# Optimization experiments

Hardware: AMD Instinct MI355X
Metric: run time of the kernel (lower is better)

Reference implementation:

```python
import jax, jax.numpy as jnp
import numpy as np

D_MODEL = 128; D_STATE = 64; HEADDIM = 32; D_CONV = 4; EXPAND = 2
D_INNER = EXPAND * D_MODEL          # 256
NHEADS = D_INNER // HEADDIM         # 8
NGROUPS = 1
D_CONV_CH = D_INNER + 2 * NGROUPS * D_STATE      # 384
D_IN_PROJ = 2 * D_INNER + 2 * NGROUPS * D_STATE + NHEADS  # 648


def _mamba2(u, Win, convw, convb, dtb, Alog, Dp, normw, Wout):
    # u: (B, L, d_model). Mamba2 forward (ngroups=1, rmsnorm gated, no in/out bias).
    B, L, _ = u.shape
    zxbcdt = u @ Win                                   # (B,L,648)
    z, xBC, dt = jnp.split(zxbcdt, [D_INNER, D_INNER + D_CONV_CH], axis=-1)
    # depthwise causal conv1d (kernel D_CONV) + SiLU
    xp = jnp.pad(xBC, ((0, 0), (D_CONV - 1, 0), (0, 0)))
    xconv = sum(xp[:, k:k + L, :] * convw[k] for k in range(D_CONV)) + convb
    xBC = jax.nn.silu(xconv)
    x, Bm, Cm = jnp.split(xBC, [D_INNER, D_INNER + NGROUPS * D_STATE], axis=-1)
    dt = jax.nn.softplus(dt + dtb)                     # (B,L,H)
    A = -jnp.exp(Alog)                                 # (H,)
    xh = x.reshape(B, L, NHEADS, HEADDIM)              # (B,L,H,P)
    dA = jnp.exp(dt * A)                               # (B,L,H)

    def step(h, inp):
        dA_t, dt_t, B_t, C_t, x_t = inp
        h = h * dA_t[:, :, None, None] + jnp.einsum('bh,bn,bhp->bhpn', dt_t, B_t, x_t)
        y = jnp.einsum('bhpn,bn->bhp', h, C_t)
        return h, y

    h0 = jnp.zeros((B, NHEADS, HEADDIM, D_STATE), dtype=u.dtype)
    xs = (jnp.moveaxis(dA, 1, 0), jnp.moveaxis(dt, 1, 0), jnp.moveaxis(Bm, 1, 0),
          jnp.moveaxis(Cm, 1, 0), jnp.moveaxis(xh, 1, 0))
    _, ys = jax.lax.scan(step, h0, xs)
    y = jnp.moveaxis(ys, 0, 1) + Dp[None, None, :, None] * xh   # skip D
    y = y.reshape(B, L, D_INNER)
    # RMSNormGated (norm_before_gate=False): rmsnorm(y * silu(z)) * weight
    y = y * jax.nn.silu(z)
    y = y * jax.lax.rsqrt(jnp.mean(y * y, axis=-1, keepdims=True) + 1e-5) * normw
    return y @ Wout


def _cross_attn(x, ctx, Wq, bq, Wk, bk, Wv, bv, Wo, bo):
    Q = x @ Wq + bq
    K = ctx @ Wk + bk
    V = ctx @ Wv + bv
    att = jax.nn.softmax(jnp.einsum('bqd,bkd->bqk', Q, K) * (D_MODEL ** -0.5), axis=-1)
    return jnp.einsum('bqk,bkd->bqd', att, V) @ Wo + bo


def setup_inputs() -> dict:
    key = jax.random.key(0)
    ks = jax.random.split(key, 8)
    B, L = 2048, 8

    def lin(k, fi, fo):
        return jax.random.normal(k, (fi, fo), jnp.float32) / np.sqrt(fi)

    def mamba_params(kseq):
        k = jax.random.split(kseq, 6)
        dt = jax.random.uniform(k[3], (NHEADS,), minval=0.001, maxval=0.1)
        return {
            'Win': lin(k[0], D_MODEL, D_IN_PROJ),
            'convw': jax.random.normal(k[1], (D_CONV, D_CONV_CH), jnp.float32) * 0.2,
            'convb': jnp.zeros((D_CONV_CH,), jnp.float32),
            'dtb': dt + jnp.log(-jnp.expm1(-dt)),  # inverse softplus
            'Alog': jnp.log(jax.random.uniform(k[4], (NHEADS,), minval=1.0, maxval=16.0)),
            'D': jnp.ones((NHEADS,), jnp.float32),
            'normw': jnp.ones((D_INNER,), jnp.float32),
            'Wout': lin(k[5], D_INNER, D_MODEL),
        }

    inp = {
        'st_feature': jax.random.normal(ks[0], (B, L, D_MODEL), jnp.float32),
        'exp_feature': jax.random.normal(ks[1], (B, L, D_MODEL), jnp.float32),
    }
    for pref, p in (('st_', mamba_params(ks[2])), ('ex_', mamba_params(ks[3]))):
        for n, v in p.items():
            inp[pref + n] = v

    def ca(kseq, pref):
        k = jax.random.split(kseq, 4)
        d = {}
        for n, kk in zip(('Wq', 'Wk', 'Wv', 'Wo'), k):
            d[pref + n] = lin(kk, D_MODEL, D_MODEL)
            d[pref + 'b' + n[1]] = jnp.zeros((D_MODEL,), jnp.float32)
        return d

    inp.update(ca(ks[4], 'cx_'))  # cross_atten_exp
    inp.update(ca(ks[5], 'cs_'))  # cross_atten_st
    inp['mlp_W'] = lin(ks[6], 8 * 2 * D_MODEL, 1024)
    inp['mlp_b'] = jnp.zeros((1024,), jnp.float32)
    return inp


def reference(st_feature, exp_feature,
              st_Win, st_convw, st_convb, st_dtb, st_Alog, st_D, st_normw, st_Wout,
              ex_Win, ex_convw, ex_convb, ex_dtb, ex_Alog, ex_D, ex_normw, ex_Wout,
              cx_Wq, cx_bq, cx_Wk, cx_bk, cx_Wv, cx_bv, cx_Wo, cx_bo,
              cs_Wq, cs_bq, cs_Wk, cs_bk, cs_Wv, cs_bv, cs_Wo, cs_bo,
              mlp_W, mlp_b):
    exp_f = _mamba2(exp_feature, ex_Win, ex_convw, ex_convb, ex_dtb, ex_Alog, ex_D, ex_normw, ex_Wout)
    st_f = _mamba2(st_feature, st_Win, st_convw, st_convb, st_dtb, st_Alog, st_D, st_normw, st_Wout)
    exp_a = _cross_attn(exp_f, st_f, cx_Wq, cx_bq, cx_Wk, cx_bk, cx_Wv, cx_bv, cx_Wo, cx_bo)
    st_a = _cross_attn(st_f, exp_f, cs_Wq, cs_bq, cs_Wk, cs_bk, cs_Wv, cs_bv, cs_Wo, cs_bo)
    x = jnp.concatenate([st_a, exp_a], axis=-1)        # (B, 8, 256)
    x = x.reshape(x.shape[0], -1)                      # (B, 2048)
    return x @ mlp_W + mlp_b
```

## Files before the change

kernel.cpp:

```cpp
#include <hip/hip_runtime.h>
#include <hip/hip_bf16.h>
#include <math.h>

#define B_SZ 2048
#define L_SEQ 8
#define DMODEL 128
#define DSTATE 64
#define HEADDIM 32
#define DCONV 4
#define DINNER 256
#define NHEADS 8
#define DCONVCH 384
#define DINPROJ 648
#define NPAD 656

typedef short bf16x8 __attribute__((ext_vector_type(8)));
typedef float floatx4 __attribute__((ext_vector_type(4)));

__device__ __forceinline__ float siluf(float x) {
    return x / (1.f + expf(-x));
}
__device__ __forceinline__ float bf2f(unsigned short h) {
    unsigned int u = ((unsigned int)h) << 16;
    return __builtin_bit_cast(float, u);
}
__device__ __forceinline__ unsigned short f2bf(float f) {
    __hip_bfloat16 b = __float2bfloat16(f);
    return __builtin_bit_cast(unsigned short, b);
}
__device__ __forceinline__ void unpack8(bf16x8 v, float* o) {
    #pragma unroll
    for (int j = 0; j < 8; ++j) o[j] = bf2f((unsigned short)v[j]);
}
__device__ __forceinline__ void gl_lds16(const unsigned short* g, unsigned short* l) {
    __builtin_amdgcn_global_load_lds(
        (const __attribute__((address_space(1))) unsigned int*)g,
        (__attribute__((address_space(3))) unsigned int*)l, 16, 0, 0);
}

__global__ __launch_bounds__(256) void prep_weights(
    const float* __restrict__ st_Win, const float* __restrict__ ex_Win,
    const float* __restrict__ st_Wout, const float* __restrict__ ex_Wout,
    const float* __restrict__ st_normw, const float* __restrict__ ex_normw,
    const float* __restrict__ cs_Wq, const float* __restrict__ cs_Wk,
    const float* __restrict__ cs_Wv, const float* __restrict__ cs_Wo,
    const float* __restrict__ cx_Wq, const float* __restrict__ cx_Wk,
    const float* __restrict__ cx_Wv, const float* __restrict__ cx_Wo,
    unsigned short* __restrict__ winT_st, unsigned short* __restrict__ winT_ex,
    unsigned short* __restrict__ woutT_st, unsigned short* __restrict__ woutT_ex,
    unsigned short* __restrict__ attnWT)
{
    int blk = blockIdx.x;
    if (blk < 656) {
        const float* src = blk < 328 ? st_Win : ex_Win;
        unsigned short* dst = blk < 328 ? winT_st : winT_ex;
        int idx = (blk % 328) * 256 + threadIdx.x;
        if (idx >= NPAD * 128) return;
        int n = idx / 128, k = idx % 128;
        float v = (n < DINPROJ) ? src[k * DINPROJ + n] : 0.f;
        dst[idx] = f2bf(v);
    } else if (blk < 912) {
        const float* src = blk < 784 ? st_Wout : ex_Wout;
        const float* nw  = blk < 784 ? st_normw : ex_normw;
        unsigned short* dst = blk < 784 ? woutT_st : woutT_ex;
        int idx = ((blk - 656) % 128) * 256 + threadIdx.x;
        int n = idx / 256, k = idx % 256;
        dst[idx] = f2bf(src[k * 128 + n] * nw[k]);
    } else {
        int b2 = blk - 912;
        int mat = b2 >> 6;
        const float* src = mat == 0 ? cs_Wq : mat == 1 ? cs_Wk : mat == 2 ? cs_Wv :
                           mat == 3 ? cs_Wo : mat == 4 ? cx_Wq : mat == 5 ? cx_Wk :
                           mat == 6 ? cx_Wv : cx_Wo;
        int e = (b2 & 63) * 256 + threadIdx.x;
        int n = e >> 7, k = e & 127;
        attnWT[mat * 16384 + n * 128 + k] = f2bf(src[k * 128 + n]);
    }
}

#define LDK 136
#define LDZ 648
__global__ __launch_bounds__(256, 3) void mamba_dual(
    const float* __restrict__ u_ex, const float* __restrict__ u_st,
    const unsigned short* __restrict__ WinT_ex, const unsigned short* __restrict__ WinT_st,
    const float* __restrict__ convw_ex, const float* __restrict__ convw_st,
    const float* __restrict__ convb_ex, const float* __restrict__ convb_st,
    const float* __restrict__ dtb_ex, const float* __restrict__ dtb_st,
    const float* __restrict__ Alog_ex, const float* __restrict__ Alog_st,
    const float* __restrict__ Dp_ex, const float* __restrict__ Dp_st,
    const unsigned short* __restrict__ WoutT_ex, const unsigned short* __restrict__ WoutT_st,
    unsigned short* __restrict__ out_ex, unsigned short* __restrict__ out_st,
    const float* __restrict__ mlp_W, unsigned short* __restrict__ mlpWt)
{
    const int tid = threadIdx.x;

    __shared__ __align__(16) unsigned short uA[32 * LDK];
    __shared__ __align__(16) unsigned short zx[32 * LDZ];
    __shared__ float dtv[4][8][8];
    __shared__ float cum[4][8][8];
    __shared__ float Gm[4][8][8];

    if (blockIdx.x >= 1024) {
        int b2 = blockIdx.x - 1024;
        int n0 = (b2 & 31) * 32, k0 = (b2 >> 5) * 32;
        float* tile = (float*)uA;
        const int c = tid & 31, r0 = tid >> 5;
        for (int rr = r0; rr < 32; rr += 8)
            tile[rr * 33 + c] = mlp_W[(size_t)(k0 + rr) * 1024 + n0 + c];
        __syncthreads();
        for (int rr = r0; rr < 32; rr += 8)
            mlpWt[(size_t)(n0 + rr) * 2048 + k0 + c] = f2bf(tile[c * 33 + rr]);
        return;
    }

    const int which = blockIdx.x >> 9;
    const float* u = which ? u_st : u_ex;
    const unsigned short* WinT = which ? WinT_st : WinT_ex;
    const float* convw = which ? convw_st : convw_ex;
    const float* convb = which ? convb_st : convb_ex;
    const float* dtb = which ? dtb_st : dtb_ex;
    const float* Alog = which ? Alog_st : Alog_ex;
    const float* Dp = which ? Dp_st : Dp_ex;
    const unsigned short* WoutT = which ? WoutT_st : WoutT_ex;
    unsigned short* outf = which ? out_st : out_ex;

    const int lane = tid & 63;
    const int wave = tid >> 6;
    const int l15 = lane & 15;
    const int q8 = (lane >> 4) * 8;
    const int row0 = (lane >> 4) * 4;
    const int grow0 = (blockIdx.x & 511) * 32;

    float* coefp = (float*)uA;
    float* rstdp = coefp + 2048;

    #pragma unroll
    for (int it = 0; it < 4; ++it) {
        int i = tid + it * 256;
        int r = i >> 5, k4 = (i & 31) * 4;
        float4 v = *(const float4*)(u + (size_t)(grow0 + r) * DMODEL + k4);
        ushort4 h;
        h.x = f2bf(v.x); h.y = f2bf(v.y); h.z = f2bf(v.z); h.w = f2bf(v.w);
        *(ushort4*)(uA + r * LDK + k4) = h;
    }
    __syncthreads();

    {
        bf16x8 af[2][4];
        #pragma unroll
        for (int mt = 0; mt < 2; ++mt)
            #pragma unroll
            for (int kk = 0; kk < 4; ++kk)
                af[mt][kk] = *(const bf16x8*)(uA + (mt * 16 + l15) * LDK + kk * 32 + q8);
        for (int j = wave; j < 82; j += 4) {
            int mt = (j >= 41) ? 1 : 0;
            int nt = j - mt * 41;
            floatx4 acc = {0.f, 0.f, 0.f, 0.f};
            const unsigned short* bp = WinT + (size_t)(nt * 16 + l15) * 128 + q8;
            #pragma unroll
            for (int kk = 0; kk < 4; ++kk) {
                bf16x8 bf = *(const bf16x8*)(bp + kk * 32);
                acc = __builtin_amdgcn_mfma_f32_16x16x32_bf16(af[mt][kk], bf, acc, 0, 0, 0);
            }
            if (nt == 40) {
                if (l15 < 8) {
                    float dbv = dtb[l15];
                    #pragma unroll
                    for (int r = 0; r < 4; ++r) {
                        int rr = mt * 16 + row0 + r;
                        float v = acc[r] + dbv;
                        dtv[rr >> 3][rr & 7][l15] = (v > 20.f) ? v : log1pf(expf(v));
                    }
                }
            } else {
                #pragma unroll
                for (int r = 0; r < 4; ++r)
                    zx[(mt * 16 + row0 + r) * LDZ + nt * 16 + l15] = f2bf(acc[r]);
            }
        }
    }
    __syncthreads();

    float cv[6][8];
    {
        #pragma unroll
        for (int it = 0; it < 6; ++it) {
            int i = tid + it * 256;
            int r = i / 48, g = i % 48;
            int c0 = g * 8;
            int l = r & 7, bloc = r >> 3;
            float s[8];
            float4 cb0 = *(const float4*)(convb + c0);
            float4 cb1 = *(const float4*)(convb + c0 + 4);
            s[0] = cb0.x; s[1] = cb0.y; s[2] = cb0.z; s[3] = cb0.w;
            s[4] = cb1.x; s[5] = cb1.y; s[6] = cb1.z; s[7] = cb1.w;
            #pragma unroll
            for (int k = 0; k < DCONV; ++k) {
                int lp = l + k - (DCONV - 1);
                if (lp >= 0) {
                    bf16x8 v = *(const bf16x8*)(zx + (bloc * 8 + lp) * LDZ + 256 + c0);
                    float vf[8];
                    unpack8(v, vf);
                    float4 w0 = *(const float4*)(convw + k * DCONVCH + c0);
                    float4 w1 = *(const float4*)(convw + k * DCONVCH + c0 + 4);
                    s[0] += vf[0] * w0.x; s[1] += vf[1] * w0.y;
                    s[2] += vf[2] * w0.z; s[3] += vf[3] * w0.w;
                    s[4] += vf[4] * w1.x; s[5] += vf[5] * w1.y;
                    s[6] += vf[6] * w1.z; s[7] += vf[7] * w1.w;
                }
            }
            #pragma unroll
            for (int j = 0; j < 8; ++j) cv[it][j] = siluf(s[j]);
        }
    }
    __syncthreads();
    {
        #pragma unroll
        for (int it = 0; it < 6; ++it) {
            int i = tid + it * 256;
            int r = i / 48, c0 = (i % 48) * 8;
            bf16x8 o;
            #pragma unroll
            for (int j = 0; j < 8; ++j) o[j] = (short)f2bf(cv[it][j]);
            *(bf16x8*)(zx + r * LDZ + 256 + c0) = o;
        }
        if (tid < 32) {
            int bloc = tid >> 3, h = tid & 7;
            float c = 0.f;
            for (int l = 0; l < L_SEQ; ++l) { c += dtv[bloc][l][h]; cum[bloc][l][h] = c; }
        }
    }
    __syncthreads();

    {
        int bloc = tid >> 6, t = (tid >> 3) & 7, s = tid & 7;
        float a = 0.f;
        #pragma unroll
        for (int n = 0; n < DSTATE; n += 8) {
            bf16x8 bv = *(const bf16x8*)(zx + (bloc * 8 + s) * LDZ + 512 + n);
            bf16x8 cvv = *(const bf16x8*)(zx + (bloc * 8 + t) * LDZ + 576 + n);
            float bf_[8], cf_[8];
            unpack8(bv, bf_); unpack8(cvv, cf_);
            #pragma unroll
            for (int j = 0; j < 8; ++j) a += bf_[j] * cf_[j];
        }
        Gm[bloc][t][s] = a;
    }
    __syncthreads();

    #pragma unroll
    for (int it = 0; it < 8; ++it) {
        int i = tid + it * 256;
        int bloc = i >> 9, t = (i >> 6) & 7, s = (i >> 3) & 7, h = i & 7;
        float A = -expf(Alog[h]);
        coefp[i] = (s <= t)
            ? Gm[bloc][t][s] * expf(A * (cum[bloc][t][h] - cum[bloc][s][h])) * dtv[bloc][s][h]
            : 0.f;
    }
    __syncthreads();

    float pj[4];
    bf16x8 yo[4];
    int rF[4], c0F[4];
    {
        #pragma unroll
        for (int it = 0; it < 4; ++it) {
            int i = tid + it * 256;
            int r = i >> 5, g = i & 31;
            int c0 = g * 8, h = g >> 2;
            int bloc = r >> 3, t = r & 7;
            float acc[8];
            {
                bf16x8 xv = *(const bf16x8*)(zx + r * LDZ + 256 + c0);
                float xf[8]; unpack8(xv, xf);
                float d = Dp[h];
                #pragma unroll
                for (int j = 0; j < 8; ++j) acc[j] = d * xf[j];
            }
            for (int s = 0; s <= t; ++s) {
                float cf = coefp[((bloc * 8 + t) * 8 + s) * 8 + h];
                bf16x8 xv = *(const bf16x8*)(zx + (bloc * 8 + s) * LDZ + 256 + c0);
                float xf[8]; unpack8(xv, xf);
                #pragma unroll
                for (int j = 0; j < 8; ++j) acc[j] += cf * xf[j];
            }
            bf16x8 zv = *(const bf16x8*)(zx + r * LDZ + c0);
            float zf[8]; unpack8(zv, zf);
            float p = 0.f;
            #pragma unroll
            for (int j = 0; j < 8; ++j) {
                float y = acc[j] * siluf(zf[j]);
                p += y * y;
                yo[it][j] = (short)f2bf(y);
            }
            pj[it] = p; rF[it] = r; c0F[it] = c0;
        }
    }
    #pragma unroll
    for (int m = 1; m < 32; m <<= 1) {
        #pragma unroll
        for (int it = 0; it < 4; ++it) pj[it] += __shfl_xor(pj[it], m);
    }
    if ((tid & 31) == 0) {
        #pragma unroll
        for (int it = 0; it < 4; ++it)
            rstdp[rF[it]] = rsqrtf(pj[it] * (1.f / 256.f) + 1e-5f);
    }
    __syncthreads();
    #pragma unroll
    for (int it = 0; it < 4; ++it)
        *(bf16x8*)(zx + rF[it] * LDZ + 256 + c0F[it]) = yo[it];
    __syncthreads();

    {
        bf16x8 af[2][8];
        #pragma unroll
        for (int mt = 0; mt < 2; ++mt)
            #pragma unroll
            for (int kk = 0; kk < 8; ++kk)
                af[mt][kk] = *(const bf16x8*)(zx + (mt * 16 + l15) * LDZ + 256 + kk * 32 + q8);
        #pragma unroll
        for (int ni = 0; ni < 2; ++ni) {
            int nt = wave * 2 + ni;
            const unsigned short* bp = WoutT + (size_t)(nt * 16 + l15) * 256 + q8;
            bf16x8 bfr[8];
            #pragma unroll
            for (int kk = 0; kk < 8; ++kk) bfr[kk] = *(const bf16x8*)(bp + kk * 32);
            #pragma unroll
            for (int mt = 0; mt < 2; ++mt) {
                floatx4 acc = {0.f, 0.f, 0.f, 0.f};
                #pragma unroll
                for (int kk = 0; kk < 8; ++kk)
                    acc = __builtin_amdgcn_mfma_f32_16x16x32_bf16(af[mt][kk], bfr[kk], acc, 0, 0, 0);
                #pragma unroll
                for (int r = 0; r < 4; ++r) {
                    int rr = mt * 16 + row0 + r;
                    outf[(size_t)(grow0 + rr) * DMODEL + nt * 16 + l15] =
                        f2bf(acc[r] * rstdp[rr]);
                }
            }
        }
    }
}

#define ASTR 136
#define VSTR 40
#define PSTR 40
__global__ __launch_bounds__(256, 2) void attn_kernel(
    const unsigned short* __restrict__ st_f,
    const unsigned short* __restrict__ exp_f,
    const unsigned short* __restrict__ WT,
    const float* __restrict__ cs_bq, const float* __restrict__ cs_bk,
    const float* __restrict__ cs_bv, const float* __restrict__ cs_bo,
    const float* __restrict__ cx_bq, const float* __restrict__ cx_bk,
    const float* __restrict__ cx_bv, const float* __restrict__ cx_bo,
    __hip_bfloat16* __restrict__ x)
{
    const int tid = threadIdx.x;
    const int lane = tid & 63, wave = tid >> 6;
    const int l15 = lane & 15;
    const int q8 = (lane >> 4) * 8;
    const int row0 = (lane >> 4) * 4;
    const int grow0 = blockIdx.x * 32;
    const int b0 = blockIdx.x * 4;
    const float scale = 0.08838834764831845f;

    __shared__ __align__(16) unsigned short stf[32 * ASTR];
    __shared__ __align__(16) unsigned short exf[32 * ASTR];
    __shared__ __align__(16) unsigned short Qs[32 * ASTR];
    __shared__ __align__(16) unsigned short Ks[32 * ASTR];
    __shared__ __align__(16) unsigned short attv[32 * ASTR];
    __shared__ __align__(16) unsigned short Vt[128 * VSTR];
    __shared__ __align__(16) unsigned short P[32 * PSTR];
    __shared__ float Ss[32][33];

    #pragma unroll
    for (int it = 0; it < 2; ++it) {
        int i = tid + it * 256;
        int r = i >> 4, c8 = (i & 15) * 8;
        *(uint4*)(stf + r * ASTR + c8) = *(const uint4*)(st_f + (size_t)(grow0 + r) * 128 + c8);
        *(uint4*)(exf + r * ASTR + c8) = *(const uint4*)(exp_f + (size_t)(grow0 + r) * 128 + c8);
    }
    __syncthreads();

    #pragma unroll
    for (int pass = 0; pass < 2; ++pass) {
        const unsigned short* qsrc = pass ? exf : stf;
        const unsigned short* kvsrc = pass ? stf : exf;
        const unsigned short* Wq = WT + (size_t)pass * 4 * 16384;
        const unsigned short* Wk = Wq + 16384;
        const unsigned short* Wv = Wq + 32768;
        const unsigned short* Wo = Wq + 49152;
        const float* bq = pass ? cx_bq : cs_bq;
        const float* bk = pass ? cx_bk : cs_bk;
        const float* bv = pass ? cx_bv : cs_bv;
        const float* bo = pass ? cx_bo : cs_bo;

        {
            bf16x8 aq[2][4], akv[2][4];
            #pragma unroll
            for (int mt = 0; mt < 2; ++mt)
                #pragma unroll
                for (int kk = 0; kk < 4; ++kk) {
                    aq[mt][kk]  = *(const bf16x8*)(qsrc  + (mt * 16 + l15) * ASTR + kk * 32 + q8);
                    akv[mt][kk] = *(const bf16x8*)(kvsrc + (mt * 16 + l15) * ASTR + kk * 32 + q8);
                }
            #pragma unroll
            for (int ni = 0; ni < 2; ++ni) {
                int nc = (wave * 2 + ni) * 16 + l15;
                floatx4 aq0 = {0,0,0,0}, aq1 = {0,0,0,0};
                floatx4 ak0 = {0,0,0,0}, ak1 = {0,0,0,0};
                floatx4 av0 = {0,0,0,0}, av1 = {0,0,0,0};
                #pragma unroll
                for (int kk = 0; kk < 4; ++kk) {
                    bf16x8 wqf = *(const bf16x8*)(Wq + (size_t)nc * 128 + kk * 32 + q8);
                    bf16x8 wkf = *(const bf16x8*)(Wk + (size_t)nc * 128 + kk * 32 + q8);
                    bf16x8 wvf = *(const bf16x8*)(Wv + (size_t)nc * 128 + kk * 32 + q8);
                    aq0 = __builtin_amdgcn_mfma_f32_16x16x32_bf16(aq[0][kk],  wqf, aq0, 0, 0, 0);
                    aq1 = __builtin_amdgcn_mfma_f32_16x16x32_bf16(aq[1][kk],  wqf, aq1, 0, 0, 0);
                    ak0 = __builtin_amdgcn_mfma_f32_16x16x32_bf16(akv[0][kk], wkf, ak0, 0, 0, 0);
                    ak1 = __builtin_amdgcn_mfma_f32_16x16x32_bf16(akv[1][kk], wkf, ak1, 0, 0, 0);
                    av0 = __builtin_amdgcn_mfma_f32_16x16x32_bf16(akv[0][kk], wvf, av0, 0, 0, 0);
                    av1 = __builtin_amdgcn_mfma_f32_16x16x32_bf16(akv[1][kk], wvf, av1, 0, 0, 0);
                }
                float bqv = bq[nc], bkv = bk[nc], bvv = bv[nc];
                #pragma unroll
                for (int r = 0; r < 4; ++r) {
                    Qs[(row0 + r) * ASTR + nc]      = f2bf(aq0[r] + bqv);
                    Qs[(16 + row0 + r) * ASTR + nc] = f2bf(aq1[r] + bqv);
                    Ks[(row0 + r) * ASTR + nc]      = f2bf(ak0[r] + bkv);
                    Ks[(16 + row0 + r) * ASTR + nc] = f2bf(ak1[r] + bkv);
                    Vt[nc * VSTR + row0 + r]        = f2bf(av0[r] + bvv);
                    Vt[nc * VSTR + 16 + row0 + r]   = f2bf(av1[r] + bvv);
                }
            }
        }
        __syncthreads();

        {
            int mtS = wave >> 1, ntS = wave & 1;
            floatx4 s = {0,0,0,0};
            #pragma unroll
            for (int kk = 0; kk < 4; ++kk) {
                bf16x8 a = *(const bf16x8*)(Qs + (mtS * 16 + l15) * ASTR + kk * 32 + q8);
                bf16x8 b = *(const bf16x8*)(Ks + (ntS * 16 + l15) * ASTR + kk * 32 + q8);
                s = __builtin_amdgcn_mfma_f32_16x16x32_bf16(a, b, s, 0, 0, 0);
            }
            #pragma unroll
            for (int r = 0; r < 4; ++r)
                Ss[mtS * 16 + row0 + r][ntS * 16 + l15] = s[r];
        }
        __syncthreads();

        if (tid < 32) {
            int r = tid, c0 = (r >> 3) * 8;
            float v[8], mx = -1e30f;
            #pragma unroll
            for (int c = 0; c < 8; ++c) {
                v[c] = Ss[r][c0 + c] * scale;
                mx = fmaxf(mx, v[c]);
            }
            float sum = 0.f;
            #pragma unroll
            for (int c = 0; c < 8; ++c) { v[c] = expf(v[c] - mx); sum += v[c]; }
            float inv = 1.f / sum;
            #pragma unroll
            for (int c = 0; c < 32; ++c) {
                float pv = (c >= c0 && c < c0 + 8) ? v[c - c0] * inv : 0.f;
                P[r * PSTR + c] = f2bf(pv);
            }
        }
        __syncthreads();

        {
            #pragma unroll
            for (int ni = 0; ni < 2; ++ni) {
                int nc = (wave * 2 + ni) * 16 + l15;
                bf16x8 bv_ = *(const bf16x8*)(Vt + nc * VSTR + q8);
                #pragma unroll
                for (int mt = 0; mt < 2; ++mt) {
                    bf16x8 ap = *(const bf16x8*)(P + (mt * 16 + l15) * PSTR + q8);
                    floatx4 o = {0,0,0,0};
                    o = __builtin_amdgcn_mfma_f32_16x16x32_bf16(ap, bv_, o, 0, 0, 0);
                    #pragma unroll
                    for (int r = 0; r < 4; ++r)
                        attv[(mt * 16 + row0 + r) * ASTR + nc] = f2bf(o[r]);
                }
            }
        }
        __syncthreads();

        {
            bf16x8 ao[2][4];
            #pragma unroll
            for (int mt = 0; mt < 2; ++mt)
                #pragma unroll
                for (int kk = 0; kk < 4; ++kk)
                    ao[mt][kk] = *(const bf16x8*)(attv + (mt * 16 + l15) * ASTR + kk * 32 + q8);
            #pragma unroll
            for (int ni = 0; ni < 2; ++ni) {
                int nc = (wave * 2 + ni) * 16 + l15;
                floatx4 a0 = {0,0,0,0}, a1 = {0,0,0,0};
                #pragma unroll
                for (int kk = 0; kk < 4; ++kk) {
                    bf16x8 wof = *(const bf16x8*)(Wo + (size_t)nc * 128 + kk * 32 + q8);
                    a0 = __builtin_amdgcn_mfma_f32_16x16x32_bf16(ao[0][kk], wof, a0, 0, 0, 0);
                    a1 = __builtin_amdgcn_mfma_f32_16x16x32_bf16(ao[1][kk], wof, a1, 0, 0, 0);
                }
                float bov = bo[nc];
                #pragma unroll
                for (int r = 0; r < 4; ++r) {
                    int rr0 = row0 + r;
                    int rr1 = 16 + row0 + r;
                    x[(size_t)(b0 + (rr0 >> 3)) * 2048 + (rr0 & 7) * 256 + pass * 128 + nc] =
                        __float2bfloat16(a0[r] + bov);
                    x[(size_t)(b0 + (rr1 >> 3)) * 2048 + (rr1 & 7) * 256 + pass * 128 + nc] =
                        __float2bfloat16(a1[r] + bov);
                }
            }
        }
        __syncthreads();
    }
}

__global__ __launch_bounds__(256, 5) void mlp_mfma(
    const unsigned short* __restrict__ X,
    const unsigned short* __restrict__ Wt,
    const float* __restrict__ bias,
    float* __restrict__ out)
{
    __shared__ __align__(16) unsigned short As[2][64 * 64];
    __shared__ __align__(16) unsigned short Bs[2][64 * 64];
    const int tid = threadIdx.x;
    const int wave = tid >> 6, lane = tid & 63;
    const int wm = (wave >> 1) * 32, wn = (wave & 1) * 32;
    const int bm = blockIdx.y * 64, bn = blockIdx.x * 64;
    const int l15 = lane & 15, q8 = (lane >> 4) * 8;

    const int c0i = tid, c1i = tid + 256;
    const int r0s = c0i >> 3, c0s = ((c0i & 7) ^ (r0s & 7)) * 8;
    const int r1s = c1i >> 3, c1s = ((c1i & 7) ^ (r1s & 7)) * 8;
    const unsigned short* gA0 = X + (size_t)(bm + r0s) * 2048 + c0s;
    const unsigned short* gA1 = X + (size_t)(bm + r1s) * 2048 + c1s;
    const unsigned short* gB0 = Wt + (size_t)(bn + r0s) * 2048 + c0s;
    const unsigned short* gB1 = Wt + (size_t)(bn + r1s) * 2048 + c1s;

    floatx4 acc[2][2];
    #pragma unroll
    for (int i = 0; i < 2; ++i)
        #pragma unroll
        for (int j = 0; j < 2; ++j) acc[i][j] = (floatx4){0.f, 0.f, 0.f, 0.f};

    const int ra0 = wm + l15, ra1 = wm + 16 + l15;
    const int rb0 = wn + l15, rb1 = wn + 16 + l15;

    gl_lds16(gA0, As[0] + c0i * 8);
    gl_lds16(gA1, As[0] + c1i * 8);
    gl_lds16(gB0, Bs[0] + c0i * 8);
    gl_lds16(gB1, Bs[0] + c1i * 8);
    __syncthreads();

    int cur = 0;
    for (int t = 0; t < 32; ++t) {
        if (t < 31) {
            int k0 = (t + 1) * 64;
            unsigned short* An = As[cur ^ 1];
            unsigned short* Bn = Bs[cur ^ 1];
            gl_lds16(gA0 + k0, An + c0i * 8);
            gl_lds16(gA1 + k0, An + c1i * 8);
            gl_lds16(gB0 + k0, Bn + c0i * 8);
            gl_lds16(gB1 + k0, Bn + c1i * 8);
        }
        const unsigned short* Ac = As[cur];
        const unsigned short* Bc = Bs[cur];
        #pragma unroll
        for (int ks = 0; ks < 2; ++ks) {
            int xx = ks * 4 + (q8 >> 3);
            bf16x8 a0 = *(const bf16x8*)(Ac + (ra0 * 8 + (xx ^ (ra0 & 7))) * 8);
            bf16x8 a1 = *(const bf16x8*)(Ac + (ra1 * 8 + (xx ^ (ra1 & 7))) * 8);
            bf16x8 b0 = *(const bf16x8*)(Bc + (rb0 * 8 + (xx ^ (rb0 & 7))) * 8);
            bf16x8 b1 = *(const bf16x8*)(Bc + (rb1 * 8 + (xx ^ (rb1 & 7))) * 8);
            acc[0][0] = __builtin_amdgcn_mfma_f32_16x16x32_bf16(a0, b0, acc[0][0], 0, 0, 0);
            acc[0][1] = __builtin_amdgcn_mfma_f32_16x16x32_bf16(a0, b1, acc[0][1], 0, 0, 0);
            acc[1][0] = __builtin_amdgcn_mfma_f32_16x16x32_bf16(a1, b0, acc[1][0], 0, 0, 0);
            acc[1][1] = __builtin_amdgcn_mfma_f32_16x16x32_bf16(a1, b1, acc[1][1], 0, 0, 0);
        }
        __syncthreads();
        cur ^= 1;
    }

    const int row0 = (lane >> 4) * 4;
    #pragma unroll
    for (int j = 0; j < 2; ++j) {
        int col = bn + wn + j * 16 + l15;
        float bv = bias[col];
        #pragma unroll
        for (int r = 0; r < 4; ++r) {
            out[(size_t)(bm + wm + row0 + r) * 1024 + col] = acc[0][j][r] + bv;
            out[(size_t)(bm + wm + 16 + row0 + r) * 1024 + col] = acc[1][j][r] + bv;
        }
    }
}

extern "C" void kernel_launch(void* const* d_in, const int* in_sizes, int n_in,
                              void* d_out, int out_size, void* d_ws, size_t ws_size,
                              hipStream_t stream) {
    const float* st_feature = (const float*)d_in[0];
    const float* exp_feature = (const float*)d_in[1];
    const float* st_Win = (const float*)d_in[2];
    const float* st_convw = (const float*)d_in[3];
    const float* st_convb = (const float*)d_in[4];
    const float* st_dtb = (const float*)d_in[5];
    const float* st_Alog = (const float*)d_in[6];
    const float* st_D = (const float*)d_in[7];
    const float* st_normw = (const float*)d_in[8];
    const float* st_Wout = (const float*)d_in[9];
    const float* ex_Win = (const float*)d_in[10];
    const float* ex_convw = (const float*)d_in[11];
    const float* ex_convb = (const float*)d_in[12];
    const float* ex_dtb = (const float*)d_in[13];
    const float* ex_Alog = (const float*)d_in[14];
    const float* ex_D = (const float*)d_in[15];
    const float* ex_normw = (const float*)d_in[16];
    const float* ex_Wout = (const float*)d_in[17];
    const float* cx_Wq = (const float*)d_in[18]; const float* cx_bq = (const float*)d_in[19];
    const float* cx_Wk = (const float*)d_in[20]; const float* cx_bk = (const float*)d_in[21];
    const float* cx_Wv = (const float*)d_in[22]; const float* cx_bv = (const float*)d_in[23];
    const float* cx_Wo = (const float*)d_in[24]; const float* cx_bo = (const float*)d_in[25];
    const float* cs_Wq = (const float*)d_in[26]; const float* cs_bq = (const float*)d_in[27];
    const float* cs_Wk = (const float*)d_in[28]; const float* cs_bk = (const float*)d_in[29];
    const float* cs_Wv = (const float*)d_in[30]; const float* cs_bv = (const float*)d_in[31];
    const float* cs_Wo = (const float*)d_in[32]; const float* cs_bo = (const float*)d_in[33];
    const float* mlp_W = (const float*)d_in[34];
    const float* mlp_b = (const float*)d_in[35];

    unsigned short* wsu = (unsigned short*)d_ws;
    unsigned short* st_fb  = wsu;
    unsigned short* exp_fb = st_fb + (size_t)B_SZ * L_SEQ * DMODEL;
    unsigned short* xbuf   = exp_fb + (size_t)B_SZ * L_SEQ * DMODEL;
    unsigned short* wtbuf  = xbuf + (size_t)2048 * 2048;
    unsigned short* winT_st = wtbuf + (size_t)1024 * 2048;
    unsigned short* winT_ex = winT_st + (size_t)NPAD * 128;
    unsigned short* woutT_st = winT_ex + (size_t)NPAD * 128;
    unsigned short* woutT_ex = woutT_st + (size_t)128 * 256;
    unsigned short* attnWT  = woutT_ex + (size_t)128 * 256;

    prep_weights<<<1424, 256, 0, stream>>>(
        st_Win, ex_Win, st_Wout, ex_Wout, st_normw, ex_normw,
        cs_Wq, cs_Wk, cs_Wv, cs_Wo, cx_Wq, cx_Wk, cx_Wv, cx_Wo,
        winT_st, winT_ex, woutT_st, woutT_ex, attnWT);
    mamba_dual<<<3072, 256, 0, stream>>>(
        exp_feature, st_feature, winT_ex, winT_st,
        ex_convw, st_convw, ex_convb, st_convb,
        ex_dtb, st_dtb, ex_Alog, st_Alog, ex_D, st_D,
        woutT_ex, woutT_st,
        exp_fb, st_fb,
        mlp_W, wtbuf);
    attn_kernel<<<B_SZ / 4, 256, 0, stream>>>(st_fb, exp_fb, attnWT,
                                              cs_bq, cs_bk, cs_bv, cs_bo,
                                              cx_bq, cx_bk, cx_bv, cx_bo,
                                              (__hip_bfloat16*)xbuf);
    {
        dim3 g(1024 / 64, 2048 / 64);
        mlp_mfma<<<g, 256, 0, stream>>>(xbuf, wtbuf, mlp_b, (float*)d_out);
    }
}
```

Baseline: 260.7 us.

## Fuse cross-attention into Mamba kernel by pairing exp/st rows per block

Each Mamba block now handles 16 rows from the exp stream and the matching 16 rows from the st stream, so both feature sets for two batch items sit in the same block. The cross-attention (QKV projections, scores, softmax, PV and output projection) then runs inside the same kernel on shared memory. This removes the separate attention launch and the global round-trip of both feature buffers. In exchange each block switches weight pointers per half, loads Wout fragments per tile instead of reusing them across both row tiles, and does more serial work, which may raise register pressure.

After: 271.2 us. 1.04x slower.

```diff
diff --git a/kernel.cpp b/kernel.cpp
--- a/kernel.cpp
+++ b/kernel.cpp
@@ -80,7 +80,8 @@
 
 #define LDK 136
 #define LDZ 648
-__global__ __launch_bounds__(256, 3) void mamba_dual(
+#define ASTR 136
+__global__ __launch_bounds__(256, 3) void mamba_attn(
     const float* __restrict__ u_ex, const float* __restrict__ u_st,
     const unsigned short* __restrict__ WinT_ex, const unsigned short* __restrict__ WinT_st,
     const float* __restrict__ convw_ex, const float* __restrict__ convw_st,
@@ -89,7 +90,12 @@
     const float* __restrict__ Alog_ex, const float* __restrict__ Alog_st,
     const float* __restrict__ Dp_ex, const float* __restrict__ Dp_st,
     const unsigned short* __restrict__ WoutT_ex, const unsigned short* __restrict__ WoutT_st,
-    unsigned short* __restrict__ out_ex, unsigned short* __restrict__ out_st,
+    const unsigned short* __restrict__ attnWT,
+    const float* __restrict__ cs_bq, const float* __restrict__ cs_bk,
+    const float* __restrict__ cs_bv, const float* __restrict__ cs_bo,
+    const float* __restrict__ cx_bq, const float* __restrict__ cx_bk,
+    const float* __restrict__ cx_bv, const float* __restrict__ cx_bo,
+    __hip_bfloat16* __restrict__ x,
     const float* __restrict__ mlp_W, unsigned short* __restrict__ mlpWt)
 {
     const int tid = threadIdx.x;
@@ -113,32 +119,25 @@
         return;
     }
 
-    const int which = blockIdx.x >> 9;
-    const float* u = which ? u_st : u_ex;
-    const unsigned short* WinT = which ? WinT_st : WinT_ex;
-    const float* convw = which ? convw_st : convw_ex;
-    const float* convb = which ? convb_st : convb_ex;
-    const float* dtb = which ? dtb_st : dtb_ex;
-    const float* Alog = which ? Alog_st : Alog_ex;
-    const float* Dp = which ? Dp_st : Dp_ex;
-    const unsigned short* WoutT = which ? WoutT_st : WoutT_ex;
-    unsigned short* outf = which ? out_st : out_ex;
-
     const int lane = tid & 63;
     const int wave = tid >> 6;
     const int l15 = lane & 15;
     const int q8 = (lane >> 4) * 8;
     const int row0 = (lane >> 4) * 4;
-    const int grow0 = (blockIdx.x & 511) * 32;
+    const int pairIdx = blockIdx.x;
+    const int grow0 = pairIdx * 16;
+    const int b0 = pairIdx * 2;
 
     float* coefp = (float*)uA;
-    float* rstdp = coefp + 2048;
+    float* rstdp = (float*)Gm;
 
     #pragma unroll
     for (int it = 0; it < 4; ++it) {
         int i = tid + it * 256;
         int r = i >> 5, k4 = (i & 31) * 4;
-        float4 v = *(const float4*)(u + (size_t)(grow0 + r) * DMODEL + k4);
+        const float* usrc = (r < 16) ? (u_ex + (size_t)(grow0 + r) * DMODEL)
+                                     : (u_st + (size_t)(grow0 + r - 16) * DMODEL);
+        float4 v = *(const float4*)(usrc + k4);
         ushort4 h;
         h.x = f2bf(v.x); h.y = f2bf(v.y); h.z = f2bf(v.z); h.w = f2bf(v.w);
         *(ushort4*)(uA + r * LDK + k4) = h;
@@ -155,6 +154,7 @@
         for (int j = wave; j < 82; j += 4) {
             int mt = (j >= 41) ? 1 : 0;
             int nt = j - mt * 41;
+            const unsigned short* WinT = mt ? WinT_st : WinT_ex;
             floatx4 acc = {0.f, 0.f, 0.f, 0.f};
             const unsigned short* bp = WinT + (size_t)(nt * 16 + l15) * 128 + q8;
             #pragma unroll
@@ -164,7 +164,7 @@
             }
             if (nt == 40) {
                 if (l15 < 8) {
-                    float dbv = dtb[l15];
+                    float dbv = (mt ? dtb_st : dtb_ex)[l15];
                     #pragma unroll
                     for (int r = 0; r < 4; ++r) {
                         int rr = mt * 16 + row0 + r;
@@ -189,9 +189,11 @@
             int r = i / 48, g = i % 48;
             int c0 = g * 8;
             int l = r & 7, bloc = r >> 3;
+            const float* cw = (r < 16) ? convw_ex : convw_st;
+            const float* cb = (r < 16) ? convb_ex : convb_st;
             float s[8];
-            float4 cb0 = *(const float4*)(convb + c0);
-            float4 cb1 = *(const float4*)(convb + c0 + 4);
+            float4 cb0 = *(const float4*)(cb + c0);
+            float4 cb1 = *(const float4*)(cb + c0 + 4);
             s[0] = cb0.x; s[1] = cb0.y; s[2] = cb0.z; s[3] = cb0.w;
             s[4] = cb1.x; s[5] = cb1.y; s[6] = cb1.z; s[7] = cb1.w;
             #pragma unroll
@@ -201,8 +203,8 @@
                     bf16x8 v = *(const bf16x8*)(zx + (bloc * 8 + lp) * LDZ + 256 + c0);
                     float vf[8];
                     unpack8(v, vf);
-                    float4 w0 = *(const float4*)(convw + k * DCONVCH + c0);
-                    float4 w1 = *(const float4*)(convw + k * DCONVCH + c0 + 4);
+                    float4 w0 = *(const float4*)(cw + k * DCONVCH + c0);
+                    float4 w1 = *(const float4*)(cw + k * DCONVCH + c0 + 4);
                     s[0] += vf[0] * w0.x; s[1] += vf[1] * w0.y;
                     s[2] += vf[2] * w0.z; s[3] += vf[3] * w0.w;
                     s[4] += vf[4] * w1.x; s[5] += vf[5] * w1.y;
@@ -252,7 +254,7 @@
     for (int it = 0; it < 8; ++it) {
         int i = tid + it * 256;
         int bloc = i >> 9, t = (i >> 6) & 7, s = (i >> 3) & 7, h = i & 7;
-        float A = -expf(Alog[h]);
+        float A = -expf((bloc < 2 ? Alog_ex : Alog_st)[h]);
         coefp[i] = (s <= t)
             ? Gm[bloc][t][s] * expf(A * (cum[bloc][t][h] - cum[bloc][s][h])) * dtv[bloc][s][h]
             : 0.f;
@@ -273,7 +275,7 @@
             {
                 bf16x8 xv = *(const bf16x8*)(zx + r * LDZ + 256 + c0);
                 float xf[8]; unpack8(xv, xf);
-                float d = Dp[h];
+                float d = (bloc < 2 ? Dp_ex : Dp_st)[h];
                 #pragma unroll
                 for (int j = 0; j < 8; ++j) acc[j] = d * xf[j];
             }
@@ -312,6 +314,7 @@
         *(bf16x8*)(zx + rF[it] * LDZ + 256 + c0F[it]) = yo[it];
     __syncthreads();
 
+    unsigned short* fout = uA;
     {
         bf16x8 af[2][8];
         #pragma unroll
@@ -322,204 +325,156 @@
         #pragma unroll
         for (int ni = 0; ni < 2; ++ni) {
             int nt = wave * 2 + ni;
-            const unsigned short* bp = WoutT + (size_t)(nt * 16 + l15) * 256 + q8;
-            bf16x8 bfr[8];
-            #pragma unroll
-            for (int kk = 0; kk < 8; ++kk) bfr[kk] = *(const bf16x8*)(bp + kk * 32);
             #pragma unroll
             for (int mt = 0; mt < 2; ++mt) {
+                const unsigned short* WoutT = mt ? WoutT_st : WoutT_ex;
+                const unsigned short* bp = WoutT + (size_t)(nt * 16 + l15) * 256 + q8;
                 floatx4 acc = {0.f, 0.f, 0.f, 0.f};
                 #pragma unroll
-                for (int kk = 0; kk < 8; ++kk)
-                    acc = __builtin_amdgcn_mfma_f32_16x16x32_bf16(af[mt][kk], bfr[kk], acc, 0, 0, 0);
+                for (int kk = 0; kk < 8; ++kk) {
+                    bf16x8 bf = *(const bf16x8*)(bp + kk * 32);
+                    acc = __builtin_amdgcn_mfma_f32_16x16x32_bf16(af[mt][kk], bf, acc, 0, 0, 0);
+                }
                 #pragma unroll
                 for (int r = 0; r < 4; ++r) {
                     int rr = mt * 16 + row0 + r;
-                    outf[(size_t)(grow0 + rr) * DMODEL + nt * 16 + l15] =
-                        f2bf(acc[r] * rstdp[rr]);
-                }
-            }
-        }
-    }
-}
-
-#define ASTR 136
-#define VSTR 40
-#define PSTR 40
-__global__ __launch_bounds__(256, 2) void attn_kernel(
-    const unsigned short* __restrict__ st_f,
-    const unsigned short* __restrict__ exp_f,
-    const unsigned short* __restrict__ WT,
-    const float* __restrict__ cs_bq, const float* __restrict__ cs_bk,
-    const float* __restrict__ cs_bv, const float* __restrict__ cs_bo,
-    const float* __restrict__ cx_bq, const float* __restrict__ cx_bk,
-    const float* __restrict__ cx_bv, const float* __restrict__ cx_bo,
-    __hip_bfloat16* __restrict__ x)
-{
-    const int tid = threadIdx.x;
-    const int lane = tid & 63, wave = tid >> 6;
-    const int l15 = lane & 15;
-    const int q8 = (lane >> 4) * 8;
-    const int row0 = (lane >> 4) * 4;
-    const int grow0 = blockIdx.x * 32;
-    const int b0 = blockIdx.x * 4;
+                    fout[rr * ASTR + nt * 16 + l15] = f2bf(acc[r] * rstdp[rr]);
+                }
+            }
+        }
+    }
+    __syncthreads();
+
+    unsigned short* Qs  = zx;
+    unsigned short* Ks  = zx + 4352;
+    unsigned short* Vt  = zx + 8704;
+    unsigned short* P   = zx + 13824;
+    float*          Ssf = (float*)(zx + 15104);
+    unsigned short* attv = Qs;
     const float scale = 0.08838834764831845f;
 
-    __shared__ __align__(16) unsigned short stf[32 * ASTR];
-    __shared__ __align__(16) unsigned short exf[32 * ASTR];
-    __shared__ __align__(16) unsigned short Qs[32 * ASTR];
-    __shared__ __align__(16) unsigned short Ks[32 * ASTR];
-    __shared__ __align__(16) unsigned short attv[32 * ASTR];
-    __shared__ __align__(16) unsigned short Vt[128 * VSTR];
-    __shared__ __align__(16) unsigned short P[32 * PSTR];
-    __shared__ float Ss[32][33];
-
-    #pragma unroll
-    for (int it = 0; it < 2; ++it) {
-        int i = tid + it * 256;
-        int r = i >> 4, c8 = (i & 15) * 8;
-        *(uint4*)(stf + r * ASTR + c8) = *(const uint4*)(st_f + (size_t)(grow0 + r) * 128 + c8);
-        *(uint4*)(exf + r * ASTR + c8) = *(const uint4*)(exp_f + (size_t)(grow0 + r) * 128 + c8);
-    }
-    __syncthreads();
-
-    #pragma unroll
-    for (int pass = 0; pass < 2; ++pass) {
-        const unsigned short* qsrc = pass ? exf : stf;
-        const unsigned short* kvsrc = pass ? stf : exf;
-        const unsigned short* Wq = WT + (size_t)pass * 4 * 16384;
-        const unsigned short* Wk = Wq + 16384;
-        const unsigned short* Wv = Wq + 32768;
-        const unsigned short* Wo = Wq + 49152;
-        const float* bq = pass ? cx_bq : cs_bq;
-        const float* bk = pass ? cx_bk : cs_bk;
-        const float* bv = pass ? cx_bv : cs_bv;
-        const float* bo = pass ? cx_bo : cs_bo;
-
-        {
-            bf16x8 aq[2][4], akv[2][4];
-            #pragma unroll
-            for (int mt = 0; mt < 2; ++mt)
-                #pragma unroll
-                for (int kk = 0; kk < 4; ++kk) {
-                    aq[mt][kk]  = *(const bf16x8*)(qsrc  + (mt * 16 + l15) * ASTR + kk * 32 + q8);
-                    akv[mt][kk] = *(const bf16x8*)(kvsrc + (mt * 16 + l15) * ASTR + kk * 32 + q8);
-                }
+    {
+        #pragma unroll
+        for (int pass = 0; pass < 2; ++pass) {
+            const unsigned short* qsrc  = pass ? fout : (fout + 16 * ASTR);
+            const unsigned short* kvsrc = pass ? (fout + 16 * ASTR) : fout;
+            const unsigned short* Wq = attnWT + (size_t)pass * 4 * 16384;
+            const unsigned short* Wk = Wq + 16384;
+            const unsigned short* Wv = Wq + 32768;
+            const float* bq = pass ? cx_bq : cs_bq;
+            const float* bk = pass ? cx_bk : cs_bk;
+            const float* bv = pass ? cx_bv : cs_bv;
+            bf16x8 aq[4], akv[4];
+            #pragma unroll
+            for (int kk = 0; kk < 4; ++kk) {
+                aq[kk]  = *(const bf16x8*)(qsrc  + l15 * ASTR + kk * 32 + q8);
+                akv[kk] = *(const bf16x8*)(kvsrc + l15 * ASTR + kk * 32 + q8);
+            }
             #pragma unroll
             for (int ni = 0; ni < 2; ++ni) {
                 int nc = (wave * 2 + ni) * 16 + l15;
-                floatx4 aq0 = {0,0,0,0}, aq1 = {0,0,0,0};
-                floatx4 ak0 = {0,0,0,0}, ak1 = {0,0,0,0};
-                floatx4 av0 = {0,0,0,0}, av1 = {0,0,0,0};
+                floatx4 aq0 = {0,0,0,0}, ak0 = {0,0,0,0}, av0 = {0,0,0,0};
                 #pragma unroll
                 for (int kk = 0; kk < 4; ++kk) {
                     bf16x8 wqf = *(const bf16x8*)(Wq + (size_t)nc * 128 + kk * 32 + q8);
                     bf16x8 wkf = *(const bf16x8*)(Wk + (size_t)nc * 128 + kk * 32 + q8);
                     bf16x8 wvf = *(const bf16x8*)(Wv + (size_t)nc * 128 + kk * 32 + q8);
-                    aq0 = __builtin_amdgcn_mfma_f32_16x16x32_bf16(aq[0][kk],  wqf, aq0, 0, 0, 0);
-                    aq1 = __builtin_amdgcn_mfma_f32_16x16x32_bf16(aq[1][kk],  wqf, aq1, 0, 0, 0);
-                    ak0 = __builtin_amdgcn_mfma_f32_16x16x32_bf16(akv[0][kk], wkf, ak0, 0, 0, 0);
-                    ak1 = __builtin_amdgcn_mfma_f32_16x16x32_bf16(akv[1][kk], wkf, ak1, 0, 0, 0);
-                    av0 = __builtin_amdgcn_mfma_f32_16x16x32_bf16(akv[0][kk], wvf, av0, 0, 0, 0);
-                    av1 = __builtin_amdgcn_mfma_f32_16x16x32_bf16(akv[1][kk], wvf, av1, 0, 0, 0);
+                    aq0 = __builtin_amdgcn_mfma_f32_16x16x32_bf16(aq[kk],  wqf, aq0, 0, 0, 0);
+                    ak0 = __builtin_amdgcn_mfma_f32_16x16x32_bf16(akv[kk], wkf, ak0, 0, 0, 0);
+                    av0 = __builtin_amdgcn_mfma_f32_16x16x32_bf16(akv[kk], wvf, av0, 0, 0, 0);
                 }
                 float bqv = bq[nc], bkv = bk[nc], bvv = bv[nc];
                 #pragma unroll
                 for (int r = 0; r < 4; ++r) {
-                    Qs[(row0 + r) * ASTR + nc]      = f2bf(aq0[r] + bqv);
-                    Qs[(16 + row0 + r) * ASTR + nc] = f2bf(aq1[r] + bqv);
-                    Ks[(row0 + r) * ASTR + nc]      = f2bf(ak0[r] + bkv);
-                    Ks[(16 + row0 + r) * ASTR + nc] = f2bf(ak1[r] + bkv);
-                    Vt[nc * VSTR + row0 + r]        = f2bf(av0[r] + bvv);
-                    Vt[nc * VSTR + 16 + row0 + r]   = f2bf(av1[r] + bvv);
-                }
-            }
-        }
-        __syncthreads();
-
-        {
-            int mtS = wave >> 1, ntS = wave & 1;
-            floatx4 s = {0,0,0,0};
-            #pragma unroll
-            for (int kk = 0; kk < 4; ++kk) {
-                bf16x8 a = *(const bf16x8*)(Qs + (mtS * 16 + l15) * ASTR + kk * 32 + q8);
-                bf16x8 b = *(const bf16x8*)(Ks + (ntS * 16 + l15) * ASTR + kk * 32 + q8);
-                s = __builtin_amdgcn_mfma_f32_16x16x32_bf16(a, b, s, 0, 0, 0);
-            }
-            #pragma unroll
-            for (int r = 0; r < 4; ++r)
-                Ss[mtS * 16 + row0 + r][ntS * 16 + l15] = s[r];
-        }
-        __syncthreads();
-
-        if (tid < 32) {
-            int r = tid, c0 = (r >> 3) * 8;
-            float v[8], mx = -1e30f;
-            #pragma unroll
-            for (int c = 0; c < 8; ++c) {
-                v[c] = Ss[r][c0 + c] * scale;
-                mx = fmaxf(mx, v[c]);
-            }
-            float sum = 0.f;
-            #pragma unroll
-            for (int c = 0; c < 8; ++c) { v[c] = expf(v[c] - mx); sum += v[c]; }
-            float inv = 1.f / sum;
-            #pragma unroll
-            for (int c = 0; c < 32; ++c) {
-                float pv = (c >= c0 && c < c0 + 8) ? v[c - c0] * inv : 0.f;
-                P[r * PSTR + c] = f2bf(pv);
-            }
-        }
-        __syncthreads();
-
-        {
+                    Qs[(pass * 16 + row0 + r) * ASTR + nc] = f2bf(aq0[r] + bqv);
+                    Ks[(pass * 16 + row0 + r) * ASTR + nc] = f2bf(ak0[r] + bkv);
+                    Vt[nc * 40 + pass * 16 + row0 + r]     = f2bf(av0[r] + bvv);
+                }
+            }
+        }
+    }
+    __syncthreads();
+
+    if (wave < 2) {
+        int pass = wave;
+        floatx4 s = {0,0,0,0};
+        #pragma unroll
+        for (int kk = 0; kk < 4; ++kk) {
+            bf16x8 a = *(const bf16x8*)(Qs + (pass * 16 + l15) * ASTR + kk * 32 + q8);
+            bf16x8 b = *(const bf16x8*)(Ks + (pass * 16 + l15) * ASTR + kk * 32 + q8);
+            s = __builtin_amdgcn_mfma_f32_16x16x32_bf16(a, b, s, 0, 0, 0);
+        }
+        #pragma unroll
+        for (int r = 0; r < 4; ++r)
+            Ssf[(pass * 16 + row0 + r) * 17 + l15] = s[r];
+    }
+    __syncthreads();
+
+    if (tid < 32) {
+        int pass = tid >> 4, r = tid & 15, c0 = (r >> 3) * 8;
+        float v[8], mx = -1e30f;
+        #pragma unroll
+        for (int c = 0; c < 8; ++c) {
+            v[c] = Ssf[(pass * 16 + r) * 17 + c0 + c] * scale;
+            mx = fmaxf(mx, v[c]);
+        }
+        float sum = 0.f;
+        #pragma unroll
+        for (int c = 0; c < 8; ++c) { v[c] = expf(v[c] - mx); sum += v[c]; }
+        float inv = 1.f / sum;
+        #pragma unroll
+        for (int c = 0; c < 32; ++c) {
+            float pv = (c >= c0 && c < c0 + 8) ? v[c - c0] * inv : 0.f;
+            P[(pass * 16 + r) * 40 + c] = f2bf(pv);
+        }
+    }
+    __syncthreads();
+
+    {
+        #pragma unroll
+        for (int pass = 0; pass < 2; ++pass) {
             #pragma unroll
             for (int ni = 0; ni < 2; ++ni) {
                 int nc = (wave * 2 + ni) * 16 + l15;
-                bf16x8 bv_ = *(const bf16x8*)(Vt + nc * VSTR + q8);
-                #pragma unroll
-                for (int mt = 0; mt < 2; ++mt) {
-                    bf16x8 ap = *(const bf16x8*)(P + (mt * 16 + l15) * PSTR + q8);
-                    floatx4 o = {0,0,0,0};
-                    o = __builtin_amdgcn_mfma_f32_16x16x32_bf16(ap, bv_, o, 0, 0, 0);
-                    #pragma unroll
-                    for (int r = 0; r < 4; ++r)
-                        attv[(mt * 16 + row0 + r) * ASTR + nc] = f2bf(o[r]);
-                }
-            }
-        }
-        __syncthreads();
-
-        {
-            bf16x8 ao[2][4];
-            #pragma unroll
-            for (int mt = 0; mt < 2; ++mt)
-                #pragma unroll
-                for (int kk = 0; kk < 4; ++kk)
-                    ao[mt][kk] = *(const bf16x8*)(attv + (mt * 16 + l15) * ASTR + kk * 32 + q8);
+                bf16x8 bv_ = *(const bf16x8*)(Vt + nc * 40 + pass * 16 + q8);
+                bf16x8 ap = *(const bf16x8*)(P + (pass * 16 + l15) * 40 + q8);
+                floatx4 o = {0,0,0,0};
+                o = __builtin_amdgcn_mfma_f32_16x16x32_bf16(ap, bv_, o, 0, 0, 0);
+                #pragma unroll
+                for (int r = 0; r < 4; ++r)
+                    attv[(pass * 16 + row0 + r) * ASTR + nc] = f2bf(o[r]);
+            }
+        }
+    }
+    __syncthreads();
+
+    {
+        #pragma unroll
+        for (int pass = 0; pass < 2; ++pass) {
+            const unsigned short* Wo = attnWT + (size_t)pass * 4 * 16384 + 49152;
+            const float* bo = pass ? cx_bo : cs_bo;
+            bf16x8 ao[4];
+            #pragma unroll
+            for (int kk = 0; kk < 4; ++kk)
+                ao[kk] = *(const bf16x8*)(attv + (pass * 16 + l15) * ASTR + kk * 32 + q8);
             #pragma unroll
             for (int ni = 0; ni < 2; ++ni) {
                 int nc = (wave * 2 + ni) * 16 + l15;
-                floatx4 a0 = {0,0,0,0}, a1 = {0,0,0,0};
+                floatx4 a0 = {0,0,0,0};
                 #pragma unroll
                 for (int kk = 0; kk < 4; ++kk) {
                     bf16x8 wof = *(const bf16x8*)(Wo + (size_t)nc * 128 + kk * 32 + q8);
-                    a0 = __builtin_amdgcn_mfma_f32_16x16x32_bf16(ao[0][kk], wof, a0, 0, 0, 0);
-                    a1 = __builtin_amdgcn_mfma_f32_16x16x32_bf16(ao[1][kk], wof, a1, 0, 0, 0);
+                    a0 = __builtin_amdgcn_mfma_f32_16x16x32_bf16(ao[kk], wof, a0, 0, 0, 0);
                 }
                 float bov = bo[nc];
                 #pragma unroll
                 for (int r = 0; r < 4; ++r) {
-                    int rr0 = row0 + r;
-                    int rr1 = 16 + row0 + r;
-                    x[(size_t)(b0 + (rr0 >> 3)) * 2048 + (rr0 & 7) * 256 + pass * 128 + nc] =
+                    int rr = row0 + r;
+                    x[(size_t)(b0 + (rr >> 3)) * 2048 + (rr & 7) * 256 + pass * 128 + nc] =
                         __float2bfloat16(a0[r] + bov);
-                    x[(size_t)(b0 + (rr1 >> 3)) * 2048 + (rr1 & 7) * 256 + pass * 128 + nc] =
-                        __float2bfloat16(a1[r] + bov);
-                }
-            }
-        }
-        __syncthreads();
+                }
+            }
+        }
     }
 }
 
@@ -635,9 +590,7 @@
     const float* mlp_b = (const float*)d_in[35];
 
     unsigned short* wsu = (unsigned short*)d_ws;
-    unsigned short* st_fb  = wsu;
-    unsigned short* exp_fb = st_fb + (size_t)B_SZ * L_SEQ * DMODEL;
-    unsigned short* xbuf   = exp_fb + (size_t)B_SZ * L_SEQ * DMODEL;
+    unsigned short* xbuf   = wsu;
     unsigned short* wtbuf  = xbuf + (size_t)2048 * 2048;
     unsigned short* winT_st = wtbuf + (size_t)1024 * 2048;
     unsigned short* winT_ex = winT_st + (size_t)NPAD * 128;
@@ -649,17 +602,16 @@
         st_Win, ex_Win, st_Wout, ex_Wout, st_normw, ex_normw,
         cs_Wq, cs_Wk, cs_Wv, cs_Wo, cx_Wq, cx_Wk, cx_Wv, cx_Wo,
         winT_st, winT_ex, woutT_st, woutT_ex, attnWT);
-    mamba_dual<<<3072, 256, 0, stream>>>(
+    mamba_attn<<<3072, 256, 0, stream>>>(
         exp_feature, st_feature, winT_ex, winT_st,
         ex_convw, st_convw, ex_convb, st_convb,
         ex_dtb, st_dtb, ex_Alog, st_Alog, ex_D, st_D,
         woutT_ex, woutT_st,
-        exp_fb, st_fb,
+        attnWT,
+        cs_bq, cs_bk, cs_bv, cs_bo,
+        cx_bq, cx_bk, cx_bv, cx_bo,
+        (__hip_bfloat16*)xbuf,
         mlp_W, wtbuf);
-    attn_kernel<<<B_SZ / 4, 256, 0, stream>>>(st_fb, exp_fb, attnWT,
-                                              cs_bq, cs_bk, cs_bv, cs_bo,
-                                              cx_bq, cx_bk, cx_bv, cx_bo,
-                                              (__hip_bfloat16*)xbuf);
     {
         dim3 g(1024 / 64, 2048 / 64);
         mlp_mfma<<<g, 256, 0, stream>>>(xbuf, wtbuf, mlp_b, (float*)d_out);
```
